# Optimization experiments

Measured on AMD Instinct MI355X. Metric: run time of the kernel, lower is better.

## Reference

```python
import jax, jax.numpy as jnp
import numpy as np

N = 50000
E = 800000
IN_FEATS = 256
NUM_HEADS = 4
OUT_FEATS = 64
NUM_ETYPES = 8
ALPHA = 100.0
NEG_SLOPE_ATTN = 0.2   # self.leaky_relu
NEG_SLOPE_EW = 0.01    # nn.LeakyReLU() default, applied to edge weights


def leaky_relu(x, slope):
    return jnp.where(x >= 0, x, slope * x)


def setup_inputs() -> dict:
    key = jax.random.key(0)
    ks = jax.random.split(key, 8)
    feat = jax.random.normal(ks[0], (N, IN_FEATS), dtype=jnp.float32)
    src = jax.random.randint(ks[1], (E,), 0, N, dtype=jnp.int32)
    dst = jax.random.randint(ks[2], (E,), 0, N, dtype=jnp.int32)
    # etypes are 1-indexed in the original code (edge_weight[edge_feats - 1])
    edge_feats = jax.random.randint(ks[3], (E,), 1, NUM_ETYPES + 1, dtype=jnp.int32)
    # parameters (xavier-normal-ish init for weights; edge_weight = 1/alpha)
    fc_w = jax.random.normal(ks[4], (NUM_HEADS * OUT_FEATS, IN_FEATS), dtype=jnp.float32) * 0.05
    attn_l = jax.random.normal(ks[5], (1, NUM_HEADS, OUT_FEATS), dtype=jnp.float32) * 0.1
    attn_r = jax.random.normal(ks[6], (1, NUM_HEADS, OUT_FEATS), dtype=jnp.float32) * 0.1
    edge_weight = jnp.full((NUM_ETYPES, NUM_HEADS), 1.0 / ALPHA, dtype=jnp.float32)
    return {"feat": feat, "src": src, "dst": dst, "edge_feats": edge_feats,
            "fc_w": fc_w, "attn_l": attn_l, "attn_r": attn_r, "edge_weight": edge_weight}


def reference(feat, src, dst, edge_feats, fc_w, attn_l, attn_r, edge_weight):
    # feat: [N, F_in] -> ft: [N, H, D]
    ft = (feat @ fc_w.T).reshape(-1, NUM_HEADS, OUT_FEATS)
    el = jnp.einsum('nhd,ohd->nh', ft, attn_l)  # [N, H]
    er = jnp.einsum('nhd,ohd->nh', ft, attn_r)  # [N, H]
    # edge-type weights (1-indexed), scaled & leaky-relu'd
    ew = leaky_relu(edge_weight * ALPHA, NEG_SLOPE_EW)  # [T, H]
    ee = ew[edge_feats - 1]                              # [E, H]
    # per-edge logits: u_add_v, times edge weight, leaky relu
    e = leaky_relu((el[src] + er[dst]) * ee, NEG_SLOPE_ATTN)  # [E, H]
    # edge softmax grouped by destination node
    emax = jax.ops.segment_max(e, dst, num_segments=N)        # [N, H]
    ex = jnp.exp(e - emax[dst])
    denom = jax.ops.segment_sum(ex, dst, num_segments=N)      # [N, H]
    a = ex / denom[dst]                                        # [E, H]
    # weighted scatter-sum: sum over edges of a * ft[src]
    msg = ft[src] * a[:, :, None]                              # [E, H, D]
    rst = jax.ops.segment_sum(msg, dst, num_segments=N)       # [N, H, D]
    return rst
```

## Files before the change

kernel.cpp:

```cpp
#include <hip/hip_runtime.h>
#include <hip/hip_bf16.h>


#define NF 256
#define HD 256
#define NH 4
#define PB 256

typedef __attribute__((ext_vector_type(8))) short short8;
typedef __attribute__((ext_vector_type(4))) float f32x4;

static __device__ __forceinline__ unsigned short f2bf(float f) {
  unsigned int u = __float_as_uint(f);
  u += 0x7FFFu + ((u >> 16) & 1u);
  return (unsigned short)(u >> 16);
}
static __device__ __forceinline__ float bf2f(unsigned short s) {
  return __uint_as_float(((unsigned int)s) << 16);
}
static __device__ __forceinline__ unsigned pkbf(float a, float b) {
  __hip_bfloat162 h = __float22bfloat162_rn(make_float2(a, b));
  return *(unsigned*)&h;
}
static __device__ __forceinline__ float wcalc(float sum, float ew) {
  float x = sum * ew;
  x = (x >= 0.f) ? x : 0.2f * x;
  return __expf(x);
}

__global__ __launch_bounds__(256) void part_hist_k(
    const int* __restrict__ dst, const float* __restrict__ w,
    unsigned short* __restrict__ o, int* __restrict__ ghist, int e, int epb) {
  __shared__ int bins[256];
  int tid = threadIdx.x, blk = blockIdx.x;
  bins[tid] = 0;
  int ci = blk * 256 + tid;
  if (ci < 16384) {
    float4 v = ((const float4*)w)[ci];
    ((uint2*)o)[ci] = make_uint2(pkbf(v.x, v.y), pkbf(v.z, v.w));
  }
  __syncthreads();
  int e0 = blk * epb, e1 = e0 + epb; if (e1 > e) e1 = e;
  for (int i = e0 + tid; i < e1; i += 256)
    atomicAdd(&bins[dst[i] >> 8], 1);
  __syncthreads();
  ghist[tid * PB + blk] = bins[tid];
}

__global__ __launch_bounds__(1024) void scan2_k(const int* __restrict__ in,
                                                int* __restrict__ outp, int n) {
  __shared__ int wtot[16];
  __shared__ int wexcl[16];
  __shared__ int ctot;
  int tid = threadIdx.x, lane = tid & 63, wid = tid >> 6;
  int carry = 0;
  int nchunk = (n + 8191) >> 13;
  for (int c = 0; c < nchunk; ++c) {
    int base = (c << 13) + tid * 8;
    int v[8];
    if (base + 8 <= n) {
      int4 a = *(const int4*)(in + base);
      int4 b = *(const int4*)(in + base + 4);
      v[0] = a.x; v[1] = a.y; v[2] = a.z; v[3] = a.w;
      v[4] = b.x; v[5] = b.y; v[6] = b.z; v[7] = b.w;
    } else {
#pragma unroll
      for (int j = 0; j < 8; ++j) v[j] = (base + j < n) ? in[base + j] : 0;
    }
    int p[8]; int run = 0;
#pragma unroll
    for (int j = 0; j < 8; ++j) { run += v[j]; p[j] = run; }
    int incl = run;
#pragma unroll
    for (int off = 1; off < 64; off <<= 1) {
      int t = __shfl_up(incl, off);
      if (lane >= off) incl += t;
    }
    if (lane == 63) wtot[wid] = incl;
    __syncthreads();
    if (wid == 0 && lane < 16) {
      int wv = wtot[lane]; int wi = wv;
#pragma unroll
      for (int off = 1; off < 16; off <<= 1) {
        int t = __shfl_up(wi, off);
        if (lane >= off) wi += t;
      }
      wexcl[lane] = wi - wv;
      if (lane == 15) ctot = wi;
    }
    __syncthreads();
    int ebase = carry + wexcl[wid] + (incl - run);
#pragma unroll
    for (int j = 0; j < 8; ++j) {
      int i = base + j;
      if (i < n) outp[i] = ebase + p[j] - v[j];
    }
    carry += ctot;
    __syncthreads();
  }
  if (tid == 0) outp[n] = carry;
}

__global__ __launch_bounds__(256) void part_scatter_k(
    const int* __restrict__ src, const int* __restrict__ dst,
    const int* __restrict__ efeats, const int* __restrict__ sg,
    int* __restrict__ mid, int e, int epb) {
  __shared__ int cur[256];
  int tid = threadIdx.x, blk = blockIdx.x;
  cur[tid] = sg[tid * PB + blk];
  __syncthreads();
  int e0 = blk * epb, e1 = e0 + epb; if (e1 > e) e1 = e;
  for (int i = e0 + tid; i < e1; i += 256) {
    int d = dst[i];
    int pos = atomicAdd(&cur[d >> 8], 1);
    mid[pos] = src[i] | ((efeats[i] - 1) << 17) | ((d & 255) << 20);
  }
}

__global__ __launch_bounds__(256) void bucket_k(
    const int* __restrict__ mid, const int* __restrict__ sg,
    int* __restrict__ poffs, int* __restrict__ pk, int nN) {
  __shared__ int cnt[256];
  __shared__ int cur[256];
  int tid = threadIdx.x, b = blockIdx.x;
  int bb0 = sg[b * PB];
  int bb1 = sg[(b + 1) * PB];
  cnt[tid] = 0;
  __syncthreads();
  for (int i = bb0 + tid; i < bb1; i += 256)
    atomicAdd(&cnt[(mid[i] >> 20) & 255], 1);
  __syncthreads();
  if (tid < 64) {
    int carry = 0;
#pragma unroll
    for (int c = 0; c < 4; ++c) {
      int v = cnt[c * 64 + tid];
      int inc = v;
#pragma unroll
      for (int off = 1; off < 64; off <<= 1) {
        int t2 = __shfl_up(inc, off);
        if (tid >= off) inc += t2;
      }
      cur[c * 64 + tid] = inc - v + carry;
      carry += __shfl(inc, 63);
    }
  }
  __syncthreads();
  int node = b * 256 + tid;
  int g = bb0 + cur[tid];
  if (node <= nN) poffs[node] = g;
  cur[tid] = g;
  __syncthreads();
  for (int i = bb0 + tid; i < bb1; i += 256) {
    int v = mid[i];
    int pos = atomicAdd(&cur[(v >> 20) & 255], 1);
    pk[pos] = v & 0xFFFFF;
  }
}

__global__ __launch_bounds__(256) void gemm_k(
    const float* __restrict__ feat, const unsigned short* __restrict__ fcb,
    const float* __restrict__ attn_l, const float* __restrict__ attn_r,
    unsigned short* __restrict__ ftb, float* __restrict__ el,
    float* __restrict__ er, int n) {
  __shared__ short aF[4 * 2 * 64 * 8];
  __shared__ short bF[16 * 2 * 64 * 8];
  int tid = threadIdx.x;
  int lane = tid & 63, w = tid >> 6;
  int row0 = blockIdx.x * 64;

  f32x4 acc[4][4];
#pragma unroll
  for (int i = 0; i < 4; ++i)
#pragma unroll
    for (int j = 0; j < 4; ++j) acc[i][j] = (f32x4){0.f, 0.f, 0.f, 0.f};

  int ar = tid >> 2, ak = (tid & 3) << 4;
  int arow = row0 + ar; if (arow >= n) arow = n - 1;
  const float* ap = feat + (size_t)arow * NF + ak;
  int am = ar & 15, art = ar >> 4;
  int s0 = ak >> 5, q0 = (ak >> 3) & 3;
  int s1 = (ak + 8) >> 5, q1 = ((ak + 8) >> 3) & 3;
  short* aw0 = &aF[(((art * 2 + s0) * 64) + q0 * 16 + am) * 8];
  short* aw1 = &aF[(((art * 2 + s1) * 64) + q1 * 16 + am) * 8];

  const unsigned short* bp = fcb + (size_t)tid * NF;
  int bn = tid & 15, bcg = tid >> 4;

  for (int k0 = 0; k0 < NF; k0 += 64) {
    float4 f0 = *(const float4*)(ap + k0);
    float4 f1 = *(const float4*)(ap + k0 + 4);
    float4 f2 = *(const float4*)(ap + k0 + 8);
    float4 f3 = *(const float4*)(ap + k0 + 12);
    uint4 oa = make_uint4(pkbf(f0.x, f0.y), pkbf(f0.z, f0.w),
                          pkbf(f1.x, f1.y), pkbf(f1.z, f1.w));
    uint4 ob = make_uint4(pkbf(f2.x, f2.y), pkbf(f2.z, f2.w),
                          pkbf(f3.x, f3.y), pkbf(f3.z, f3.w));
    *(uint4*)aw0 = oa;
    *(uint4*)aw1 = ob;
#pragma unroll
    for (int o8 = 0; o8 < 8; ++o8) {
      short8 bv = *(const short8*)(bp + k0 + o8 * 8);
      int bs = o8 >> 2, bq = o8 & 3;
      *(short8*)&bF[(((bcg * 2 + bs) * 64) + bq * 16 + bn) * 8] = bv;
    }
    __syncthreads();
#pragma unroll
    for (int s = 0; s < 2; ++s) {
      short8 af[4], bfr[4];
#pragma unroll
      for (int rt = 0; rt < 4; ++rt)
        af[rt] = *(const short8*)&aF[(((rt * 2 + s) * 64) + lane) * 8];
#pragma unroll
      for (int ct = 0; ct < 4; ++ct)
        bfr[ct] = *(const short8*)&bF[((((w * 4 + ct) * 2 + s) * 64) + lane) * 8];
#pragma unroll
      for (int rt = 0; rt < 4; ++rt)
#pragma unroll
        for (int ct = 0; ct < 4; ++ct)
          acc[rt][ct] = __builtin_amdgcn_mfma_f32_16x16x32_bf16(
              af[rt], bfr[ct], acc[rt][ct], 0, 0, 0);
    }
    __syncthreads();
  }

  int ln = lane & 15, lq = lane >> 4;
  float al4[4], ar4[4];
#pragma unroll
  for (int ct = 0; ct < 4; ++ct) {
    al4[ct] = attn_l[w * 64 + ct * 16 + ln];
    ar4[ct] = attn_r[w * 64 + ct * 16 + ln];
  }
#pragma unroll
  for (int rt = 0; rt < 4; ++rt) {
#pragma unroll
    for (int r = 0; r < 4; ++r) {
      float pl = 0.f, pr = 0.f;
#pragma unroll
      for (int ct = 0; ct < 4; ++ct) {
        float v = acc[rt][ct][r];
        pl += v * al4[ct]; pr += v * ar4[ct];
      }
#pragma unroll
      for (int off = 1; off <= 8; off <<= 1) {
        pl += __shfl_xor(pl, off);
        pr += __shfl_xor(pr, off);
      }
      int row = row0 + rt * 16 + lq * 4 + r;
      if (row < n) {
        if (ln == 0) { el[row * NH + w] = pl; er[row * NH + w] = pr; }
        unsigned short* fr = ftb + (size_t)row * HD + w * 64 + ln;
#pragma unroll
        for (int ct = 0; ct < 4; ++ct) fr[ct * 16] = f2bf(acc[rt][ct][r]);
      }
    }
  }
}

__global__ __launch_bounds__(256) void agg3_k(
    const unsigned short* __restrict__ ftb, const int* __restrict__ pk,
    const float* __restrict__ el, const float* __restrict__ er,
    const float* __restrict__ ewt, const int* __restrict__ offs,
    float* __restrict__ out, int n) {
  __shared__ float ew_s[32];
  if (threadIdx.x < 32) {
    float v = ewt[threadIdx.x] * 100.0f;
    ew_s[threadIdx.x] = (v >= 0.f) ? v : 0.01f * v;
  }
  __syncthreads();
  int node = blockIdx.x * 4 + (threadIdx.x >> 6);
  int lane = threadIdx.x & 63;
  if (node >= n) return;
  int start = offs[node];
  int deg = offs[node + 1] - start;
  float o0 = 0.f, o1 = 0.f, o2 = 0.f, o3 = 0.f;
  if (deg > 0) {
    int hl = lane >> 4;
    float er_h = er[(size_t)node * NH + hl];
    const unsigned short* fb = ftb + (size_t)lane * 4;
    const float* elh = el + hl;
    const int* pg = pk + start;
    float ss = 0.f;
    int i = 0;
    for (; i + 8 <= deg; i += 8) {
      int4 pa = *(const int4*)(pg + i);
      int4 pb = *(const int4*)(pg + i + 4);
      int sA = pa.x & 0x1FFFF, tA = pa.x >> 17;
      int sB = pa.y & 0x1FFFF, tB = pa.y >> 17;
      int sC = pa.z & 0x1FFFF, tC = pa.z >> 17;
      int sD = pa.w & 0x1FFFF, tD = pa.w >> 17;
      int sE = pb.x & 0x1FFFF, tE = pb.x >> 17;
      int sF = pb.y & 0x1FFFF, tF = pb.y >> 17;
      int sG = pb.z & 0x1FFFF, tG = pb.z >> 17;
      int sH = pb.w & 0x1FFFF, tH = pb.w >> 17;
      float eA = elh[sA * NH], eB = elh[sB * NH], eC = elh[sC * NH], eD = elh[sD * NH];
      float eE = elh[sE * NH], eF = elh[sF * NH], eG = elh[sG * NH], eH = elh[sH * NH];
      ushort4 fA = *(const ushort4*)(fb + (size_t)sA * HD);
      ushort4 fB = *(const ushort4*)(fb + (size_t)sB * HD);
      ushort4 fC = *(const ushort4*)(fb + (size_t)sC * HD);
      ushort4 fD = *(const ushort4*)(fb + (size_t)sD * HD);
      ushort4 fE = *(const ushort4*)(fb + (size_t)sE * HD);
      ushort4 fF = *(const ushort4*)(fb + (size_t)sF * HD);
      ushort4 fG = *(const ushort4*)(fb + (size_t)sG * HD);
      ushort4 fH = *(const ushort4*)(fb + (size_t)sH * HD);
      float wA = wcalc(eA + er_h, ew_s[tA * NH + hl]);
      float wB = wcalc(eB + er_h, ew_s[tB * NH + hl]);
      float wC = wcalc(eC + er_h, ew_s[tC * NH + hl]);
      float wD = wcalc(eD + er_h, ew_s[tD * NH + hl]);
      float wE = wcalc(eE + er_h, ew_s[tE * NH + hl]);
      float wF = wcalc(eF + er_h, ew_s[tF * NH + hl]);
      float wG = wcalc(eG + er_h, ew_s[tG * NH + hl]);
      float wH = wcalc(eH + er_h, ew_s[tH * NH + hl]);
      ss += ((wA + wB) + (wC + wD)) + ((wE + wF) + (wG + wH));
      o0 = fmaf(wA, bf2f(fA.x), o0); o1 = fmaf(wA, bf2f(fA.y), o1);
      o2 = fmaf(wA, bf2f(fA.z), o2); o3 = fmaf(wA, bf2f(fA.w), o3);
      o0 = fmaf(wB, bf2f(fB.x), o0); o1 = fmaf(wB, bf2f(fB.y), o1);
      o2 = fmaf(wB, bf2f(fB.z), o2); o3 = fmaf(wB, bf2f(fB.w), o3);
      o0 = fmaf(wC, bf2f(fC.x), o0); o1 = fmaf(wC, bf2f(fC.y), o1);
      o2 = fmaf(wC, bf2f(fC.z), o2); o3 = fmaf(wC, bf2f(fC.w), o3);
      o0 = fmaf(wD, bf2f(fD.x), o0); o1 = fmaf(wD, bf2f(fD.y), o1);
      o2 = fmaf(wD, bf2f(fD.z), o2); o3 = fmaf(wD, bf2f(fD.w), o3);
      o0 = fmaf(wE, bf2f(fE.x), o0); o1 = fmaf(wE, bf2f(fE.y), o1);
      o2 = fmaf(wE, bf2f(fE.z), o2); o3 = fmaf(wE, bf2f(fE.w), o3);
      o0 = fmaf(wF, bf2f(fF.x), o0); o1 = fmaf(wF, bf2f(fF.y), o1);
      o2 = fmaf(wF, bf2f(fF.z), o2); o3 = fmaf(wF, bf2f(fF.w), o3);
      o0 = fmaf(wG, bf2f(fG.x), o0); o1 = fmaf(wG, bf2f(fG.y), o1);
      o2 = fmaf(wG, bf2f(fG.z), o2); o3 = fmaf(wG, bf2f(fG.w), o3);
      o0 = fmaf(wH, bf2f(fH.x), o0); o1 = fmaf(wH, bf2f(fH.y), o1);
      o2 = fmaf(wH, bf2f(fH.z), o2); o3 = fmaf(wH, bf2f(fH.w), o3);
    }
    for (; i < deg; ++i) {
      int pv = pg[i];
      int sA = pv & 0x1FFFF, tA = pv >> 17;
      float eA = elh[sA * NH];
      ushort4 fA = *(const ushort4*)(fb + (size_t)sA * HD);
      float wA = wcalc(eA + er_h, ew_s[tA * NH + hl]);
      ss += wA;
      o0 = fmaf(wA, bf2f(fA.x), o0); o1 = fmaf(wA, bf2f(fA.y), o1);
      o2 = fmaf(wA, bf2f(fA.z), o2); o3 = fmaf(wA, bf2f(fA.w), o3);
    }
    float rs = 1.0f / ss;
    o0 *= rs; o1 *= rs; o2 *= rs; o3 *= rs;
  }
  *(float4*)(out + (size_t)node * HD + lane * 4) = make_float4(o0, o1, o2, o3);
}

extern "C" void kernel_launch(void* const* d_in, const int* in_sizes, int n_in,
                              void* d_out, int out_size, void* d_ws, size_t ws_size,
                              hipStream_t stream) {
  const float* feat   = (const float*)d_in[0];
  const int*   src    = (const int*)d_in[1];
  const int*   dst    = (const int*)d_in[2];
  const int*   efeats = (const int*)d_in[3];
  const float* fc_w   = (const float*)d_in[4];
  const float* attn_l = (const float*)d_in[5];
  const float* attn_r = (const float*)d_in[6];
  const float* ewt    = (const float*)d_in[7];
  float* out = (float*)d_out;

  int N = in_sizes[0] / NF;
  int E = in_sizes[1];

  char* ws = (char*)d_ws;
  size_t off = 0;
  unsigned short* fcb = (unsigned short*)(ws + off); off += (size_t)NF * HD * 2;
  unsigned short* ftb = (unsigned short*)(ws + off); off += (size_t)N * HD * 2;
  float* el  = (float*)(ws + off);  off += (size_t)N * NH * 4;
  float* er  = (float*)(ws + off);  off += (size_t)N * NH * 4;
  int* poffs = (int*)(ws + off);    off += ((size_t)N + 16) * 4;
  int* ghist = (int*)(ws + off);    off += (size_t)PB * 256 * 4;
  int* sg    = (int*)(ws + off);    off += ((size_t)PB * 256 + 8) * 4;
  int* mid   = (int*)(ws + off);    off += (size_t)E * 4;
  int* pk    = (int*)(ws + off);    off += (size_t)E * 4;

  int epb = (E + PB - 1) / PB;
  int NB = (N >> 8) + 1;

  part_hist_k<<<PB, 256, 0, stream>>>(dst, fc_w, fcb, ghist, E, epb);
  scan2_k<<<1, 1024, 0, stream>>>(ghist, sg, PB * 256);
  part_scatter_k<<<PB, 256, 0, stream>>>(src, dst, efeats, sg, mid, E, epb);
  bucket_k<<<NB, 256, 0, stream>>>(mid, sg, poffs, pk, N);
  gemm_k<<<(N + 63) / 64, 256, 0, stream>>>(feat, fcb, attn_l, attn_r, ftb, el, er, N);
  agg3_k<<<(N + 3) / 4, 256, 0, stream>>>(ftb, pk, el, er, ewt, poffs, out, N);
}
```

Baseline: 270.7 us.

## Fuse GEMM halves into histogram and scatter kernels, simplify scan

The GEMM is split in two halves whose tiles ride as extra blocks in the histogram and scatter kernels. This overlaps the compute-bound projection with the atomic-heavy partitioning and removes separate launches. The GEMM now loads fp32 feat and fc_w straight from global memory into MFMA fragments, with no LDS staging and no pre-converted weight buffer. The scan becomes a per-bucket column scan plus a 256-wide bucket-base scan instead of one large serial scan. The trade-off is uncoalesced direct fragment loads and converting fc_w redundantly in every tile.

```diff
diff --git a/kernel.cpp b/kernel.cpp
--- a/kernel.cpp
+++ b/kernel.cpp
@@ -27,201 +27,60 @@
   x = (x >= 0.f) ? x : 0.2f * x;
   return __expf(x);
 }
-
-__global__ __launch_bounds__(256) void part_hist_k(
-    const int* __restrict__ dst, const float* __restrict__ w,
-    unsigned short* __restrict__ o, int* __restrict__ ghist, int e, int epb) {
-  __shared__ int bins[256];
-  int tid = threadIdx.x, blk = blockIdx.x;
-  bins[tid] = 0;
-  int ci = blk * 256 + tid;
-  if (ci < 16384) {
-    float4 v = ((const float4*)w)[ci];
-    ((uint2*)o)[ci] = make_uint2(pkbf(v.x, v.y), pkbf(v.z, v.w));
-  }
-  __syncthreads();
-  int e0 = blk * epb, e1 = e0 + epb; if (e1 > e) e1 = e;
-  for (int i = e0 + tid; i < e1; i += 256)
-    atomicAdd(&bins[dst[i] >> 8], 1);
-  __syncthreads();
-  ghist[tid * PB + blk] = bins[tid];
-}
-
-__global__ __launch_bounds__(1024) void scan2_k(const int* __restrict__ in,
-                                                int* __restrict__ outp, int n) {
-  __shared__ int wtot[16];
-  __shared__ int wexcl[16];
-  __shared__ int ctot;
-  int tid = threadIdx.x, lane = tid & 63, wid = tid >> 6;
-  int carry = 0;
-  int nchunk = (n + 8191) >> 13;
-  for (int c = 0; c < nchunk; ++c) {
-    int base = (c << 13) + tid * 8;
-    int v[8];
-    if (base + 8 <= n) {
-      int4 a = *(const int4*)(in + base);
-      int4 b = *(const int4*)(in + base + 4);
-      v[0] = a.x; v[1] = a.y; v[2] = a.z; v[3] = a.w;
-      v[4] = b.x; v[5] = b.y; v[6] = b.z; v[7] = b.w;
-    } else {
-#pragma unroll
-      for (int j = 0; j < 8; ++j) v[j] = (base + j < n) ? in[base + j] : 0;
-    }
-    int p[8]; int run = 0;
-#pragma unroll
-    for (int j = 0; j < 8; ++j) { run += v[j]; p[j] = run; }
-    int incl = run;
-#pragma unroll
-    for (int off = 1; off < 64; off <<= 1) {
-      int t = __shfl_up(incl, off);
-      if (lane >= off) incl += t;
-    }
-    if (lane == 63) wtot[wid] = incl;
-    __syncthreads();
-    if (wid == 0 && lane < 16) {
-      int wv = wtot[lane]; int wi = wv;
-#pragma unroll
-      for (int off = 1; off < 16; off <<= 1) {
-        int t = __shfl_up(wi, off);
-        if (lane >= off) wi += t;
-      }
-      wexcl[lane] = wi - wv;
-      if (lane == 15) ctot = wi;
-    }
-    __syncthreads();
-    int ebase = carry + wexcl[wid] + (incl - run);
-#pragma unroll
-    for (int j = 0; j < 8; ++j) {
-      int i = base + j;
-      if (i < n) outp[i] = ebase + p[j] - v[j];
-    }
-    carry += ctot;
-    __syncthreads();
-  }
-  if (tid == 0) outp[n] = carry;
-}
-
-__global__ __launch_bounds__(256) void part_scatter_k(
-    const int* __restrict__ src, const int* __restrict__ dst,
-    const int* __restrict__ efeats, const int* __restrict__ sg,
-    int* __restrict__ mid, int e, int epb) {
-  __shared__ int cur[256];
-  int tid = threadIdx.x, blk = blockIdx.x;
-  cur[tid] = sg[tid * PB + blk];
-  __syncthreads();
-  int e0 = blk * epb, e1 = e0 + epb; if (e1 > e) e1 = e;
-  for (int i = e0 + tid; i < e1; i += 256) {
-    int d = dst[i];
-    int pos = atomicAdd(&cur[d >> 8], 1);
-    mid[pos] = src[i] | ((efeats[i] - 1) << 17) | ((d & 255) << 20);
-  }
-}
-
-__global__ __launch_bounds__(256) void bucket_k(
-    const int* __restrict__ mid, const int* __restrict__ sg,
-    int* __restrict__ poffs, int* __restrict__ pk, int nN) {
-  __shared__ int cnt[256];
-  __shared__ int cur[256];
-  int tid = threadIdx.x, b = blockIdx.x;
-  int bb0 = sg[b * PB];
-  int bb1 = sg[(b + 1) * PB];
-  cnt[tid] = 0;
-  __syncthreads();
-  for (int i = bb0 + tid; i < bb1; i += 256)
-    atomicAdd(&cnt[(mid[i] >> 20) & 255], 1);
-  __syncthreads();
-  if (tid < 64) {
-    int carry = 0;
-#pragma unroll
-    for (int c = 0; c < 4; ++c) {
-      int v = cnt[c * 64 + tid];
-      int inc = v;
-#pragma unroll
-      for (int off = 1; off < 64; off <<= 1) {
-        int t2 = __shfl_up(inc, off);
-        if (tid >= off) inc += t2;
-      }
-      cur[c * 64 + tid] = inc - v + carry;
-      carry += __shfl(inc, 63);
-    }
-  }
-  __syncthreads();
-  int node = b * 256 + tid;
-  int g = bb0 + cur[tid];
-  if (node <= nN) poffs[node] = g;
-  cur[tid] = g;
-  __syncthreads();
-  for (int i = bb0 + tid; i < bb1; i += 256) {
-    int v = mid[i];
-    int pos = atomicAdd(&cur[(v >> 20) & 255], 1);
-    pk[pos] = v & 0xFFFFF;
-  }
-}
-
-__global__ __launch_bounds__(256) void gemm_k(
-    const float* __restrict__ feat, const unsigned short* __restrict__ fcb,
+static __device__ __forceinline__ short8 cvt8(float4 x, float4 y) {
+  union { short8 s; uint4 u; } cv;
+  cv.u = make_uint4(pkbf(x.x, x.y), pkbf(x.z, x.w),
+                    pkbf(y.x, y.y), pkbf(y.z, y.w));
+  return cv.s;
+}
+
+static __device__ __forceinline__ void gemm_tile_direct(
+    const float* __restrict__ feat, const float* __restrict__ fc_w,
     const float* __restrict__ attn_l, const float* __restrict__ attn_r,
     unsigned short* __restrict__ ftb, float* __restrict__ el,
-    float* __restrict__ er, int n) {
-  __shared__ short aF[4 * 2 * 64 * 8];
-  __shared__ short bF[16 * 2 * 64 * 8];
-  int tid = threadIdx.x;
+    float* __restrict__ er, int n, int row0, int tid) {
   int lane = tid & 63, w = tid >> 6;
-  int row0 = blockIdx.x * 64;
-
+  int rr = lane & 15, kq = lane >> 4;
   f32x4 acc[4][4];
 #pragma unroll
   for (int i = 0; i < 4; ++i)
 #pragma unroll
     for (int j = 0; j < 4; ++j) acc[i][j] = (f32x4){0.f, 0.f, 0.f, 0.f};
 
-  int ar = tid >> 2, ak = (tid & 3) << 4;
-  int arow = row0 + ar; if (arow >= n) arow = n - 1;
-  const float* ap = feat + (size_t)arow * NF + ak;
-  int am = ar & 15, art = ar >> 4;
-  int s0 = ak >> 5, q0 = (ak >> 3) & 3;
-  int s1 = (ak + 8) >> 5, q1 = ((ak + 8) >> 3) & 3;
-  short* aw0 = &aF[(((art * 2 + s0) * 64) + q0 * 16 + am) * 8];
-  short* aw1 = &aF[(((art * 2 + s1) * 64) + q1 * 16 + am) * 8];
-
-  const unsigned short* bp = fcb + (size_t)tid * NF;
-  int bn = tid & 15, bcg = tid >> 4;
-
-  for (int k0 = 0; k0 < NF; k0 += 64) {
-    float4 f0 = *(const float4*)(ap + k0);
-    float4 f1 = *(const float4*)(ap + k0 + 4);
-    float4 f2 = *(const float4*)(ap + k0 + 8);
-    float4 f3 = *(const float4*)(ap + k0 + 12);
-    uint4 oa = make_uint4(pkbf(f0.x, f0.y), pkbf(f0.z, f0.w),
-                          pkbf(f1.x, f1.y), pkbf(f1.z, f1.w));
-    uint4 ob = make_uint4(pkbf(f2.x, f2.y), pkbf(f2.z, f2.w),
-                          pkbf(f3.x, f3.y), pkbf(f3.z, f3.w));
-    *(uint4*)aw0 = oa;
-    *(uint4*)aw1 = ob;
-#pragma unroll
-    for (int o8 = 0; o8 < 8; ++o8) {
-      short8 bv = *(const short8*)(bp + k0 + o8 * 8);
-      int bs = o8 >> 2, bq = o8 & 3;
-      *(short8*)&bF[(((bcg * 2 + bs) * 64) + bq * 16 + bn) * 8] = bv;
-    }
-    __syncthreads();
-#pragma unroll
-    for (int s = 0; s < 2; ++s) {
-      short8 af[4], bfr[4];
-#pragma unroll
-      for (int rt = 0; rt < 4; ++rt)
-        af[rt] = *(const short8*)&aF[(((rt * 2 + s) * 64) + lane) * 8];
+  const float* ap[4];
+#pragma unroll
+  for (int rt = 0; rt < 4; ++rt) {
+    int arow = row0 + rt * 16 + rr; if (arow >= n) arow = n - 1;
+    ap[rt] = feat + (size_t)arow * NF + kq * 8;
+  }
+  const float* bp[4];
+#pragma unroll
+  for (int ct = 0; ct < 4; ++ct) {
+    int bcol = w * 64 + ct * 16 + rr;
+    bp[ct] = fc_w + (size_t)bcol * NF + kq * 8;
+  }
+
+#pragma unroll 2
+  for (int kc = 0; kc < 8; ++kc) {
+    short8 afr[4], bfr[4];
+#pragma unroll
+    for (int rt = 0; rt < 4; ++rt) {
+      float4 x = *(const float4*)(ap[rt] + kc * 32);
+      float4 y = *(const float4*)(ap[rt] + kc * 32 + 4);
+      afr[rt] = cvt8(x, y);
+    }
+#pragma unroll
+    for (int ct = 0; ct < 4; ++ct) {
+      float4 x = *(const float4*)(bp[ct] + kc * 32);
+      float4 y = *(const float4*)(bp[ct] + kc * 32 + 4);
+      bfr[ct] = cvt8(x, y);
+    }
+#pragma unroll
+    for (int rt = 0; rt < 4; ++rt)
 #pragma unroll
       for (int ct = 0; ct < 4; ++ct)
-        bfr[ct] = *(const short8*)&bF[((((w * 4 + ct) * 2 + s) * 64) + lane) * 8];
-#pragma unroll
-      for (int rt = 0; rt < 4; ++rt)
-#pragma unroll
-        for (int ct = 0; ct < 4; ++ct)
-          acc[rt][ct] = __builtin_amdgcn_mfma_f32_16x16x32_bf16(
-              af[rt], bfr[ct], acc[rt][ct], 0, 0, 0);
-    }
-    __syncthreads();
+        acc[rt][ct] = __builtin_amdgcn_mfma_f32_16x16x32_bf16(
+            afr[rt], bfr[ct], acc[rt][ct], 0, 0, 0);
   }
 
   int ln = lane & 15, lq = lane >> 4;
@@ -254,6 +113,132 @@
         for (int ct = 0; ct < 4; ++ct) fr[ct * 16] = f2bf(acc[rt][ct][r]);
       }
     }
+  }
+}
+
+__global__ __launch_bounds__(256) void hist_gemm_k(
+    const int* __restrict__ dst, int* __restrict__ ghist, int e, int epb, int hb,
+    const float* __restrict__ feat, const float* __restrict__ fc_w,
+    const float* __restrict__ attn_l, const float* __restrict__ attn_r,
+    unsigned short* __restrict__ ftb, float* __restrict__ el,
+    float* __restrict__ er, int n, int tile0) {
+  int tid = threadIdx.x;
+  if (blockIdx.x < hb) {
+    __shared__ int bins[256];
+    int blk = blockIdx.x;
+    bins[tid] = 0;
+    __syncthreads();
+    int e0 = blk * epb, e1 = e0 + epb; if (e1 > e) e1 = e;
+    for (int i = e0 + tid; i < e1; i += 256)
+      atomicAdd(&bins[dst[i] >> 8], 1);
+    __syncthreads();
+    ghist[blk * 256 + tid] = bins[tid];
+    return;
+  }
+  gemm_tile_direct(feat, fc_w, attn_l, attn_r, ftb, el, er, n,
+                   (tile0 + (int)blockIdx.x - hb) * 64, tid);
+}
+
+__global__ __launch_bounds__(256) void scan_k(
+    const int* __restrict__ ghist, int* __restrict__ lsg,
+    int* __restrict__ bb, int nblk) {
+  int tid = threadIdx.x;
+  int run = 0;
+  int i = 0;
+  for (; i + 8 <= nblk; i += 8) {
+    int v[8];
+#pragma unroll
+    for (int j = 0; j < 8; ++j) v[j] = ghist[(i + j) * 256 + tid];
+#pragma unroll
+    for (int j = 0; j < 8; ++j) { lsg[(i + j) * 256 + tid] = run; run += v[j]; }
+  }
+  for (; i < nblk; ++i) {
+    int v = ghist[i * 256 + tid];
+    lsg[i * 256 + tid] = run;
+    run += v;
+  }
+  __shared__ int wt[4];
+  int lane = tid & 63, wid = tid >> 6;
+  int inc = run;
+#pragma unroll
+  for (int off = 1; off < 64; off <<= 1) {
+    int t = __shfl_up(inc, off);
+    if (lane >= off) inc += t;
+  }
+  if (lane == 63) wt[wid] = inc;
+  __syncthreads();
+  int base = 0;
+  if (wid > 0) base += wt[0];
+  if (wid > 1) base += wt[1];
+  if (wid > 2) base += wt[2];
+  bb[tid] = base + inc - run;
+  if (tid == 255) bb[256] = base + inc;
+}
+
+__global__ __launch_bounds__(256) void scat_gemm_k(
+    const int* __restrict__ src, const int* __restrict__ dst,
+    const int* __restrict__ efeats, const int* __restrict__ lsg,
+    const int* __restrict__ bb, int* __restrict__ mid, int e, int epb, int sb,
+    const float* __restrict__ feat, const float* __restrict__ fc_w,
+    const float* __restrict__ attn_l, const float* __restrict__ attn_r,
+    unsigned short* __restrict__ ftb, float* __restrict__ el,
+    float* __restrict__ er, int n, int tile0) {
+  int tid = threadIdx.x;
+  if (blockIdx.x < sb) {
+    __shared__ int cur[256];
+    int blk = blockIdx.x;
+    cur[tid] = bb[tid] + lsg[blk * 256 + tid];
+    __syncthreads();
+    int e0 = blk * epb, e1 = e0 + epb; if (e1 > e) e1 = e;
+    for (int i = e0 + tid; i < e1; i += 256) {
+      int d = dst[i];
+      int pos = atomicAdd(&cur[d >> 8], 1);
+      mid[pos] = src[i] | ((efeats[i] - 1) << 17) | ((d & 255) << 20);
+    }
+    return;
+  }
+  gemm_tile_direct(feat, fc_w, attn_l, attn_r, ftb, el, er, n,
+                   (tile0 + (int)blockIdx.x - sb) * 64, tid);
+}
+
+__global__ __launch_bounds__(256) void bucket_k(
+    const int* __restrict__ mid, const int* __restrict__ bb,
+    int* __restrict__ poffs, int* __restrict__ pk, int nN) {
+  __shared__ int cnt[256];
+  __shared__ int cur[256];
+  int tid = threadIdx.x, b = blockIdx.x;
+  int bb0 = bb[b];
+  int bb1 = bb[b + 1];
+  cnt[tid] = 0;
+  __syncthreads();
+  for (int i = bb0 + tid; i < bb1; i += 256)
+    atomicAdd(&cnt[(mid[i] >> 20) & 255], 1);
+  __syncthreads();
+  if (tid < 64) {
+    int carry = 0;
+#pragma unroll
+    for (int c = 0; c < 4; ++c) {
+      int v = cnt[c * 64 + tid];
+      int inc = v;
+#pragma unroll
+      for (int off = 1; off < 64; off <<= 1) {
+        int t2 = __shfl_up(inc, off);
+        if (tid >= off) inc += t2;
+      }
+      cur[c * 64 + tid] = inc - v + carry;
+      carry += __shfl(inc, 63);
+    }
+  }
+  __syncthreads();
+  int node = b * 256 + tid;
+  int g = bb0 + cur[tid];
+  if (node <= nN) poffs[node] = g;
+  cur[tid] = g;
+  __syncthreads();
+  for (int i = bb0 + tid; i < bb1; i += 256) {
+    int v = mid[i];
+    int pos = atomicAdd(&cur[(v >> 20) & 255], 1);
+    pk[pos] = v & 0xFFFFF;
   }
 }
 
@@ -363,23 +348,30 @@
 
   char* ws = (char*)d_ws;
   size_t off = 0;
-  unsigned short* fcb = (unsigned short*)(ws + off); off += (size_t)NF * HD * 2;
   unsigned short* ftb = (unsigned short*)(ws + off); off += (size_t)N * HD * 2;
   float* el  = (float*)(ws + off);  off += (size_t)N * NH * 4;
   float* er  = (float*)(ws + off);  off += (size_t)N * NH * 4;
   int* poffs = (int*)(ws + off);    off += ((size_t)N + 16) * 4;
   int* ghist = (int*)(ws + off);    off += (size_t)PB * 256 * 4;
-  int* sg    = (int*)(ws + off);    off += ((size_t)PB * 256 + 8) * 4;
+  int* lsg   = (int*)(ws + off);    off += (size_t)PB * 256 * 4;
+  int* bb    = (int*)(ws + off);    off += 260 * 4;
   int* mid   = (int*)(ws + off);    off += (size_t)E * 4;
   int* pk    = (int*)(ws + off);    off += (size_t)E * 4;
 
+  int gb = (N + 63) / 64;
+  int g1 = gb / 2;
+  int g2 = gb - g1;
   int epb = (E + PB - 1) / PB;
-  int NB = (N >> 8) + 1;
-
-  part_hist_k<<<PB, 256, 0, stream>>>(dst, fc_w, fcb, ghist, E, epb);
-  scan2_k<<<1, 1024, 0, stream>>>(ghist, sg, PB * 256);
-  part_scatter_k<<<PB, 256, 0, stream>>>(src, dst, efeats, sg, mid, E, epb);
-  bucket_k<<<NB, 256, 0, stream>>>(mid, sg, poffs, pk, N);
-  gemm_k<<<(N + 63) / 64, 256, 0, stream>>>(feat, fcb, attn_l, attn_r, ftb, el, er, N);
+  int nbuck = (N + 255) >> 8;
+
+  hist_gemm_k<<<PB + g1, 256, 0, stream>>>(dst, ghist, E, epb, PB,
+                                           feat, fc_w, attn_l, attn_r,
+                                           ftb, el, er, N, 0);
+  scan_k<<<1, 256, 0, stream>>>(ghist, lsg, bb, PB);
+  scat_gemm_k<<<PB + g2, 256, 0, stream>>>(src, dst, efeats, lsg, bb, mid,
+                                           E, epb, PB,
+                                           feat, fc_w, attn_l, attn_r,
+                                           ftb, el, er, N, g1);
+  bucket_k<<<nbuck, 256, 0, stream>>>(mid, bb, poffs, pk, N);
   agg3_k<<<(N + 3) / 4, 256, 0, stream>>>(ftb, pk, el, er, ewt, poffs, out, N);
 }
```

Result: slower. 283.9 us (+4.9%).
